# Optimization experiments

Hardware: AMD Instinct MI355X
Metric: run time of the kernel (lower is better)

The kernel has to match this reference:

```python
import jax, jax.numpy as jnp
import numpy as np

NUM_USERS = 100000
NUM_ITEMS = 50000
EMBED = 64
S_NNZ = NUM_USERS * 32   # avg social degree 32
R_NNZ = NUM_USERS * 50   # avg 50 rated items per user
BATCH = 8192


def setup_inputs() -> dict:
    key = jax.random.key(0)
    ks = jax.random.split(key, 12)
    d = EMBED
    # Embedding tables (xavier-uniform style scale)
    U = jax.random.uniform(ks[0], (NUM_USERS, d), jnp.float32, -1.0, 1.0) * np.sqrt(6.0 / (NUM_USERS + d))
    V = jax.random.uniform(ks[1], (NUM_ITEMS, d), jnp.float32, -1.0, 1.0) * np.sqrt(6.0 / (NUM_ITEMS + d))
    # Diffusion layer weights: Linear(2d -> d). Stored as [2d, d] (x @ W + b).
    lim = np.sqrt(6.0 / (3 * d))
    W0 = jax.random.uniform(ks[2], (2 * d, d), jnp.float32, -lim, lim)
    b0 = jnp.zeros((d,), jnp.float32)
    W1 = jax.random.uniform(ks[3], (2 * d, d), jnp.float32, -lim, lim)
    b1 = jnp.zeros((d,), jnp.float32)
    # Sparse social matrix S [NUM_USERS, NUM_USERS], COO edge lists, row-normalized values.
    S_row = jax.random.randint(ks[4], (S_NNZ,), 0, NUM_USERS, jnp.int32)
    S_col = jax.random.randint(ks[5], (S_NNZ,), 0, NUM_USERS, jnp.int32)
    S_val = jnp.full((S_NNZ,), 1.0 / 32.0, jnp.float32)
    # Sparse rating matrix R [NUM_USERS, NUM_ITEMS]
    R_row = jax.random.randint(ks[6], (R_NNZ,), 0, NUM_USERS, jnp.int32)
    R_col = jax.random.randint(ks[7], (R_NNZ,), 0, NUM_ITEMS, jnp.int32)
    R_val = jnp.full((R_NNZ,), 1.0 / 50.0, jnp.float32)
    batch_user = jax.random.randint(ks[8], (BATCH,), 0, NUM_USERS, jnp.int64 if jax.config.jax_enable_x64 else jnp.int32)
    batch_pos_item = jax.random.randint(ks[9], (BATCH,), 0, NUM_ITEMS, jnp.int32)
    batch_neg_item = jax.random.randint(ks[10], (BATCH,), 0, NUM_ITEMS, jnp.int32)
    return dict(batch_user=batch_user, batch_pos_item=batch_pos_item, batch_neg_item=batch_neg_item,
                U=U, V=V, W0=W0, b0=b0, W1=W1, b1=b1,
                S_row=S_row, S_col=S_col, S_val=S_val,
                R_row=R_row, R_col=R_col, R_val=R_val)


def _spmm(row, col, val, X, n_rows):
    # (sparse [n_rows, n] COO) @ X : gather + scale + segment-sum
    return jax.ops.segment_sum(val[:, None] * X[col], row, num_segments=n_rows)


def reference(batch_user, batch_pos_item, batch_neg_item, U, V, W0, b0, W1, b1,
              S_row, S_col, S_val, R_row, R_col, R_val):
    # Diffusion layers: U <- relu(concat([S @ U, U]) @ W + b)
    for W, b in ((W0, b0), (W1, b1)):
        agg = _spmm(S_row, S_col, S_val, U, NUM_USERS)          # [num_users, d]
        U = jax.nn.relu(jnp.concatenate([agg, U], axis=1) @ W + b)
    user_g = U + _spmm(R_row, R_col, R_val, V, NUM_USERS)        # [num_users, d]
    bu = user_g[batch_user]          # [B, d]
    bp = V[batch_pos_item]           # [B, d]
    bn = V[batch_neg_item]           # [B, d]
    return (bu, bp, bn)
```

## Files before the change

### kernel.cpp

```cpp
#include <hip/hip_runtime.h>
#include <hip/hip_bf16.h>

#define NUM_USERS 100000
#define NUM_ITEMS 50000
#define EMBED     64
#define S_NNZ     (NUM_USERS * 32)
#define R_NNZ     (NUM_USERS * 50)
#define BATCH     8192

#define NB    256
#define NCH   256
#define CHUNK (S_NNZ / NCH)
#define BROWS 391


__global__ __launch_bounds__(256) void k_p1hist(const int* __restrict__ rows, int* __restrict__ cnt_t) {
    __shared__ int h[NB];
    int t = threadIdx.x, b = blockIdx.x;
    h[t] = 0;
    __syncthreads();
    int base = b * CHUNK;
    for (int i = t; i < CHUNK; i += 256) atomicAdd(&h[rows[base + i] / BROWS], 1);
    __syncthreads();
    cnt_t[t * NCH + b] = h[t];
}

__global__ __launch_bounds__(1024) void k_scan1(const int* __restrict__ cnt, int* __restrict__ excl,
                                                int* __restrict__ bsums, int n) {
    __shared__ int buf[1024];
    int t = threadIdx.x;
    int i = blockIdx.x * 1024 + t;
    int x = (i < n) ? cnt[i] : 0;
    buf[t] = x;
    __syncthreads();
    for (int off = 1; off < 1024; off <<= 1) {
        int y = (t >= off) ? buf[t - off] : 0;
        __syncthreads();
        buf[t] += y;
        __syncthreads();
    }
    if (i < n) excl[i] = buf[t] - x;
    if (t == 1023) bsums[blockIdx.x] = buf[1023];
}

__global__ __launch_bounds__(1024) void k_scan2(int* __restrict__ bsums, int nb, int* __restrict__ total_slot) {
    __shared__ int buf[1024];
    int t = threadIdx.x;
    int x = (t < nb) ? bsums[t] : 0;
    buf[t] = x;
    __syncthreads();
    for (int off = 1; off < 1024; off <<= 1) {
        int y = (t >= off) ? buf[t - off] : 0;
        __syncthreads();
        buf[t] += y;
        __syncthreads();
    }
    if (t < nb) bsums[t] = buf[t] - x;
    if (t == 1023) total_slot[0] = buf[1023];
}

__global__ void k_scan3b(int* __restrict__ a, const int* __restrict__ bsums, int n) {
    int i = blockIdx.x * blockDim.x + threadIdx.x;
    if (i < n) a[i] += bsums[i >> 10];
}

__global__ __launch_bounds__(256) void k_p1scatter(const int* __restrict__ rows, const int* __restrict__ cols,
                                                   const float* __restrict__ vals, const int* __restrict__ cnt_t,
                                                   int2* __restrict__ tmpE) {
    __shared__ int cur[NB];
    int t = threadIdx.x, b = blockIdx.x;
    cur[t] = cnt_t[t * NCH + b];
    __syncthreads();
    int base = b * CHUNK;
    for (int i = t; i < CHUNK; i += 256) {
        int e  = base + i;
        int r  = rows[e];
        int bk = r / BROWS;
        int pos = atomicAdd(&cur[bk], 1);
        tmpE[pos] = make_int2(((r - bk * BROWS) << 17) | cols[e], __float_as_int(vals[e]));
    }
}

__global__ __launch_bounds__(512) void k_p2(const int2* __restrict__ tmpE, const int* __restrict__ cnt_t,
                                            int* __restrict__ rowptr, int2* __restrict__ colval) {
    __shared__ int h[512];
    __shared__ int s[512];
    __shared__ int cur[512];
    int t = threadIdx.x, k = blockIdx.x;
    int beg = cnt_t[k * NCH];
    int end = (k < NB - 1) ? cnt_t[(k + 1) * NCH] : S_NNZ;
    h[t] = 0;
    __syncthreads();
    for (int j = beg + t; j < end; j += 512) atomicAdd(&h[((unsigned)tmpE[j].x) >> 17], 1);
    __syncthreads();
    s[t] = h[t];
    __syncthreads();
    for (int off = 1; off < 512; off <<= 1) {
        int y = (t >= off) ? s[t - off] : 0;
        __syncthreads();
        s[t] += y;
        __syncthreads();
    }
    int excl = s[t] - h[t];
    int gr   = k * BROWS + t;
    if (t <= BROWS && gr <= NUM_USERS) rowptr[gr] = beg + excl;
    cur[t] = beg + excl;
    __syncthreads();
    for (int j = beg + t; j < end; j += 512) {
        int2 e  = tmpE[j];
        int pos = atomicAdd(&cur[((unsigned)e.x) >> 17], 1);
        colval[pos] = make_int2(e.x & 0x1FFFF, e.y);
    }
}

__global__ void k_cvt(const float* __restrict__ src, __hip_bfloat16* __restrict__ dst, int n) {
    int i = blockIdx.x * blockDim.x + threadIdx.x;
    if (i < n) dst[i] = __float2bfloat16(src[i]);
}

__global__ __launch_bounds__(256) void k_spmm16(const int* __restrict__ rowptr,
                                                const int2* __restrict__ colval,
                                                const __hip_bfloat16* __restrict__ X,
                                                float* __restrict__ Y, int n_rows) {
    int w    = blockIdx.x * (blockDim.x >> 6) + (threadIdx.x >> 6);
    int lane = threadIdx.x & 63;
    if (w >= n_rows) return;
    int beg = rowptr[w], end = rowptr[w + 1];
    float acc = 0.0f;
    int j    = beg;
    int jend = beg + ((end - beg) & ~7);
    for (; j < jend; j += 8) {
        int2 cv[8];
#pragma unroll
        for (int u = 0; u < 8; ++u) cv[u] = colval[j + u];
        float x[8];
#pragma unroll
        for (int u = 0; u < 8; ++u) x[u] = __bfloat162float(X[(size_t)cv[u].x * EMBED + lane]);
#pragma unroll
        for (int u = 0; u < 8; ++u) acc = fmaf(__int_as_float(cv[u].y), x[u], acc);
    }
    for (; j < end; ++j)
        acc = fmaf(__int_as_float(colval[j].y), __bfloat162float(X[(size_t)colval[j].x * EMBED + lane]), acc);
    Y[(size_t)w * EMBED + lane] = acc;
}

__global__ __launch_bounds__(256) void k_spmm_batch16(const int* __restrict__ rowptr,
                                                      const int2* __restrict__ colval,
                                                      const __hip_bfloat16* __restrict__ X,
                                                      const int* __restrict__ bu,
                                                      float* __restrict__ Agg2, int n) {
    int w    = blockIdx.x * (blockDim.x >> 6) + (threadIdx.x >> 6);
    int lane = threadIdx.x & 63;
    if (w >= n) return;
    int r   = bu[w];
    int beg = rowptr[r], end = rowptr[r + 1];
    float acc = 0.0f;
    int j    = beg;
    int jend = beg + ((end - beg) & ~7);
    for (; j < jend; j += 8) {
        int2 cv[8];
#pragma unroll
        for (int u = 0; u < 8; ++u) cv[u] = colval[j + u];
        float x[8];
#pragma unroll
        for (int u = 0; u < 8; ++u) x[u] = __bfloat162float(X[(size_t)cv[u].x * EMBED + lane]);
#pragma unroll
        for (int u = 0; u < 8; ++u) acc = fmaf(__int_as_float(cv[u].y), x[u], acc);
    }
    for (; j < end; ++j)
        acc = fmaf(__int_as_float(colval[j].y), __bfloat162float(X[(size_t)colval[j].x * EMBED + lane]), acc);
    Agg2[(size_t)w * EMBED + lane] = acc;
}


__global__ __launch_bounds__(256) void k_layer(const float* __restrict__ Agg,
                                               const float* __restrict__ Uin,
                                               float* __restrict__ Uout,
                                               __hip_bfloat16* __restrict__ Uout16,
                                               const float* __restrict__ W,
                                               const float* __restrict__ b) {
    __shared__ __align__(16) float Wt[64 * 128];
    int t = threadIdx.x;
    for (int i = t; i < 128 * 64; i += 256) {
        int k = i >> 6, c = i & 63;
        Wt[c * 128 + ((((k >> 2) ^ (c & 7)) << 2) | (k & 3))] = W[i];
    }
    int rl = __builtin_amdgcn_readfirstlane(t >> 6);
    int c  = t & 63;
    int rbase = blockIdx.x * 16 + rl * 4;
    __syncthreads();
    const float4* Wt4 = (const float4*)Wt;
    int  csw   = c & 7;
    int  cbase = c * 32;
    const float4* a0 = (const float4*)(Agg + (size_t)(rbase + 0) * EMBED);
    const float4* a1 = (const float4*)(Agg + (size_t)(rbase + 1) * EMBED);
    const float4* a2 = (const float4*)(Agg + (size_t)(rbase + 2) * EMBED);
    const float4* a3 = (const float4*)(Agg + (size_t)(rbase + 3) * EMBED);
    const float4* u0 = (const float4*)(Uin + (size_t)(rbase + 0) * EMBED);
    const float4* u1 = (const float4*)(Uin + (size_t)(rbase + 1) * EMBED);
    const float4* u2 = (const float4*)(Uin + (size_t)(rbase + 2) * EMBED);
    const float4* u3 = (const float4*)(Uin + (size_t)(rbase + 3) * EMBED);
    float bias = b[c];
    float acc0 = bias, acc1 = bias, acc2 = bias, acc3 = bias;
#pragma unroll 4
    for (int k4 = 0; k4 < 16; ++k4) {
        float4 w4 = Wt4[cbase + (k4 ^ csw)];
        float4 x0 = a0[k4], x1 = a1[k4], x2 = a2[k4], x3 = a3[k4];
        acc0 = fmaf(x0.x, w4.x, acc0); acc0 = fmaf(x0.y, w4.y, acc0); acc0 = fmaf(x0.z, w4.z, acc0); acc0 = fmaf(x0.w, w4.w, acc0);
        acc1 = fmaf(x1.x, w4.x, acc1); acc1 = fmaf(x1.y, w4.y, acc1); acc1 = fmaf(x1.z, w4.z, acc1); acc1 = fmaf(x1.w, w4.w, acc1);
        acc2 = fmaf(x2.x, w4.x, acc2); acc2 = fmaf(x2.y, w4.y, acc2); acc2 = fmaf(x2.z, w4.z, acc2); acc2 = fmaf(x2.w, w4.w, acc2);
        acc3 = fmaf(x3.x, w4.x, acc3); acc3 = fmaf(x3.y, w4.y, acc3); acc3 = fmaf(x3.z, w4.z, acc3); acc3 = fmaf(x3.w, w4.w, acc3);
    }
#pragma unroll 4
    for (int k4 = 16; k4 < 32; ++k4) {
        float4 w4 = Wt4[cbase + (k4 ^ csw)];
        float4 x0 = u0[k4 - 16], x1 = u1[k4 - 16], x2 = u2[k4 - 16], x3 = u3[k4 - 16];
        acc0 = fmaf(x0.x, w4.x, acc0); acc0 = fmaf(x0.y, w4.y, acc0); acc0 = fmaf(x0.z, w4.z, acc0); acc0 = fmaf(x0.w, w4.w, acc0);
        acc1 = fmaf(x1.x, w4.x, acc1); acc1 = fmaf(x1.y, w4.y, acc1); acc1 = fmaf(x1.z, w4.z, acc1); acc1 = fmaf(x1.w, w4.w, acc1);
        acc2 = fmaf(x2.x, w4.x, acc2); acc2 = fmaf(x2.y, w4.y, acc2); acc2 = fmaf(x2.z, w4.z, acc2); acc2 = fmaf(x2.w, w4.w, acc2);
        acc3 = fmaf(x3.x, w4.x, acc3); acc3 = fmaf(x3.y, w4.y, acc3); acc3 = fmaf(x3.z, w4.z, acc3); acc3 = fmaf(x3.w, w4.w, acc3);
    }
    float v0 = fmaxf(acc0, 0.0f), v1 = fmaxf(acc1, 0.0f), v2 = fmaxf(acc2, 0.0f), v3 = fmaxf(acc3, 0.0f);
    Uout[(size_t)(rbase + 0) * EMBED + c] = v0;
    Uout[(size_t)(rbase + 1) * EMBED + c] = v1;
    Uout[(size_t)(rbase + 2) * EMBED + c] = v2;
    Uout[(size_t)(rbase + 3) * EMBED + c] = v3;
    Uout16[(size_t)(rbase + 0) * EMBED + c] = __float2bfloat16(v0);
    Uout16[(size_t)(rbase + 1) * EMBED + c] = __float2bfloat16(v1);
    Uout16[(size_t)(rbase + 2) * EMBED + c] = __float2bfloat16(v2);
    Uout16[(size_t)(rbase + 3) * EMBED + c] = __float2bfloat16(v3);
}

__global__ __launch_bounds__(256) void k_layer_batch(const float* __restrict__ Agg2,
                                                     const float* __restrict__ Uin,
                                                     const int* __restrict__ bu,
                                                     float* __restrict__ out0,
                                                     const float* __restrict__ W,
                                                     const float* __restrict__ b) {
    __shared__ __align__(16) float Wt[64 * 128];
    int t = threadIdx.x;
    for (int i = t; i < 128 * 64; i += 256) {
        int k = i >> 6, c = i & 63;
        Wt[c * 128 + ((((k >> 2) ^ (c & 7)) << 2) | (k & 3))] = W[i];
    }
    int rl = __builtin_amdgcn_readfirstlane(t >> 6);
    int c  = t & 63;
    int sbase = blockIdx.x * 16 + rl * 4;
    int r0 = bu[sbase + 0], r1 = bu[sbase + 1], r2 = bu[sbase + 2], r3 = bu[sbase + 3];
    __syncthreads();
    const float4* Wt4 = (const float4*)Wt;
    int  csw   = c & 7;
    int  cbase = c * 32;
    const float4* a0 = (const float4*)(Agg2 + (size_t)(sbase + 0) * EMBED);
    const float4* a1 = (const float4*)(Agg2 + (size_t)(sbase + 1) * EMBED);
    const float4* a2 = (const float4*)(Agg2 + (size_t)(sbase + 2) * EMBED);
    const float4* a3 = (const float4*)(Agg2 + (size_t)(sbase + 3) * EMBED);
    const float4* u0 = (const float4*)(Uin + (size_t)r0 * EMBED);
    const float4* u1 = (const float4*)(Uin + (size_t)r1 * EMBED);
    const float4* u2 = (const float4*)(Uin + (size_t)r2 * EMBED);
    const float4* u3 = (const float4*)(Uin + (size_t)r3 * EMBED);
    float bias = b[c];
    float acc0 = bias, acc1 = bias, acc2 = bias, acc3 = bias;
#pragma unroll 4
    for (int k4 = 0; k4 < 16; ++k4) {
        float4 w4 = Wt4[cbase + (k4 ^ csw)];
        float4 x0 = a0[k4], x1 = a1[k4], x2 = a2[k4], x3 = a3[k4];
        acc0 = fmaf(x0.x, w4.x, acc0); acc0 = fmaf(x0.y, w4.y, acc0); acc0 = fmaf(x0.z, w4.z, acc0); acc0 = fmaf(x0.w, w4.w, acc0);
        acc1 = fmaf(x1.x, w4.x, acc1); acc1 = fmaf(x1.y, w4.y, acc1); acc1 = fmaf(x1.z, w4.z, acc1); acc1 = fmaf(x1.w, w4.w, acc1);
        acc2 = fmaf(x2.x, w4.x, acc2); acc2 = fmaf(x2.y, w4.y, acc2); acc2 = fmaf(x2.z, w4.z, acc2); acc2 = fmaf(x2.w, w4.w, acc2);
        acc3 = fmaf(x3.x, w4.x, acc3); acc3 = fmaf(x3.y, w4.y, acc3); acc3 = fmaf(x3.z, w4.z, acc3); acc3 = fmaf(x3.w, w4.w, acc3);
    }
#pragma unroll 4
    for (int k4 = 16; k4 < 32; ++k4) {
        float4 w4 = Wt4[cbase + (k4 ^ csw)];
        float4 x0 = u0[k4 - 16], x1 = u1[k4 - 16], x2 = u2[k4 - 16], x3 = u3[k4 - 16];
        acc0 = fmaf(x0.x, w4.x, acc0); acc0 = fmaf(x0.y, w4.y, acc0); acc0 = fmaf(x0.z, w4.z, acc0); acc0 = fmaf(x0.w, w4.w, acc0);
        acc1 = fmaf(x1.x, w4.x, acc1); acc1 = fmaf(x1.y, w4.y, acc1); acc1 = fmaf(x1.z, w4.z, acc1); acc1 = fmaf(x1.w, w4.w, acc1);
        acc2 = fmaf(x2.x, w4.x, acc2); acc2 = fmaf(x2.y, w4.y, acc2); acc2 = fmaf(x2.z, w4.z, acc2); acc2 = fmaf(x2.w, w4.w, acc2);
        acc3 = fmaf(x3.x, w4.x, acc3); acc3 = fmaf(x3.y, w4.y, acc3); acc3 = fmaf(x3.z, w4.z, acc3); acc3 = fmaf(x3.w, w4.w, acc3);
    }
    out0[(size_t)(sbase + 0) * EMBED + c] = fmaxf(acc0, 0.0f);
    out0[(size_t)(sbase + 1) * EMBED + c] = fmaxf(acc1, 0.0f);
    out0[(size_t)(sbase + 2) * EMBED + c] = fmaxf(acc2, 0.0f);
    out0[(size_t)(sbase + 3) * EMBED + c] = fmaxf(acc3, 0.0f);
}


__global__ void k_chain(const int* __restrict__ bu, int* __restrict__ head,
                        int* __restrict__ nxt, unsigned* __restrict__ bitmap, int n) {
    int i = blockIdx.x * blockDim.x + threadIdx.x;
    if (i < n) {
        int u = bu[i];
        nxt[i] = atomicExch(&head[u], i);
        atomicOr(&bitmap[u >> 5], 1u << (u & 31));
    }
}

__global__ __launch_bounds__(256) void k_rcount(const int* __restrict__ rows,
                                                const unsigned* __restrict__ bitmap,
                                                const int* __restrict__ head,
                                                int* __restrict__ cntR, int nnz) {
    int e = blockIdx.x * blockDim.x + threadIdx.x;
    if (e >= nnz) return;
    int r = rows[e];
    if ((bitmap[(unsigned)r >> 5] >> (r & 31)) & 1u)
        atomicAdd(&cntR[head[r]], 1);
}

__global__ __launch_bounds__(1024) void k_rscan(const int* __restrict__ cnt,
                                                int* __restrict__ rowptr2,
                                                int* __restrict__ cur) {
    __shared__ int buf[1024];
    int t = threadIdx.x;
    int loc[8];
    int sum = 0;
#pragma unroll
    for (int q = 0; q < 8; ++q) { loc[q] = cnt[t * 8 + q]; sum += loc[q]; }
    buf[t] = sum;
    __syncthreads();
    for (int off = 1; off < 1024; off <<= 1) {
        int y = (t >= off) ? buf[t - off] : 0;
        __syncthreads();
        buf[t] += y;
        __syncthreads();
    }
    int excl = buf[t] - sum;
#pragma unroll
    for (int q = 0; q < 8; ++q) {
        rowptr2[t * 8 + q] = excl;
        cur[t * 8 + q]     = excl;
        excl += loc[q];
    }
    if (t == 1023) rowptr2[BATCH] = excl;
}

__global__ __launch_bounds__(256) void k_rscatter(const int* __restrict__ rows,
                                                  const int* __restrict__ cols,
                                                  const float* __restrict__ vals,
                                                  const unsigned* __restrict__ bitmap,
                                                  const int* __restrict__ head,
                                                  int* __restrict__ cur,
                                                  int2* __restrict__ colval2, int nnz) {
    int e = blockIdx.x * blockDim.x + threadIdx.x;
    if (e >= nnz) return;
    int r = rows[e];
    if (!((bitmap[(unsigned)r >> 5] >> (r & 31)) & 1u)) return;
    int pos = atomicAdd(&cur[head[r]], 1);
    colval2[pos] = make_int2(cols[e], __float_as_int(vals[e]));
}

__global__ __launch_bounds__(256) void k_rspmm(const int* __restrict__ rowptr2,
                                               const int2* __restrict__ colval2,
                                               const __hip_bfloat16* __restrict__ V16,
                                               const int* __restrict__ bu,
                                               const int* __restrict__ head,
                                               const int* __restrict__ nxt,
                                               float* __restrict__ out0) {
    int s    = blockIdx.x * (blockDim.x >> 6) + (threadIdx.x >> 6);
    int lane = threadIdx.x & 63;
    if (s >= BATCH) return;
    if (head[bu[s]] != s) return;
    int beg = rowptr2[s], end = rowptr2[s + 1];
    float acc = 0.0f;
    int j    = beg;
    int jend = beg + ((end - beg) & ~7);
    for (; j < jend; j += 8) {
        int2 cv[8];
#pragma unroll
        for (int u = 0; u < 8; ++u) cv[u] = colval2[j + u];
        float x[8];
#pragma unroll
        for (int u = 0; u < 8; ++u) x[u] = __bfloat162float(V16[(size_t)cv[u].x * EMBED + lane]);
#pragma unroll
        for (int u = 0; u < 8; ++u) acc = fmaf(__int_as_float(cv[u].y), x[u], acc);
    }
    for (; j < end; ++j)
        acc = fmaf(__int_as_float(colval2[j].y), __bfloat162float(V16[(size_t)colval2[j].x * EMBED + lane]), acc);
    int slot = s;
    while (slot >= 0) {
        out0[(size_t)slot * EMBED + lane] += acc;
        slot = nxt[slot];
    }
}

__global__ void k_gather2(const float* __restrict__ V,
                          const int* __restrict__ bp, const int* __restrict__ bn,
                          float* __restrict__ out) {
    int i = blockIdx.x * blockDim.x + threadIdx.x;
    if (i >= BATCH * EMBED) return;
    int row = i >> 6, l = i & 63;
    out[BATCH * EMBED + i]     = V[(size_t)bp[row] * EMBED + l];
    out[2 * BATCH * EMBED + i] = V[(size_t)bn[row] * EMBED + l];
}


extern "C" void kernel_launch(void* const* d_in, const int* in_sizes, int n_in,
                              void* d_out, int out_size, void* d_ws, size_t ws_size,
                              hipStream_t stream) {
    const int*   batch_user = (const int*)d_in[0];
    const int*   batch_pos  = (const int*)d_in[1];
    const int*   batch_neg  = (const int*)d_in[2];
    const float* U     = (const float*)d_in[3];
    const float* V     = (const float*)d_in[4];
    const float* W0    = (const float*)d_in[5];
    const float* b0    = (const float*)d_in[6];
    const float* W1    = (const float*)d_in[7];
    const float* b1    = (const float*)d_in[8];
    const int*   S_row = (const int*)d_in[9];
    const int*   S_col = (const int*)d_in[10];
    const float* S_val = (const float*)d_in[11];
    const int*   R_row = (const int*)d_in[12];
    const int*   R_col = (const int*)d_in[13];
    const float* R_val = (const float*)d_in[14];
    float* out = (float*)d_out;

    const size_t tabElems = (size_t)NUM_USERS * EMBED;

    char* wsb = (char*)d_ws;
    size_t o = 0;
    float* A       = (float*)(wsb + o); o += tabElems * 4;
    float* B       = (float*)(wsb + o); o += tabElems * 4;
    float* Agg2    = (float*)(wsb + o); o += (size_t)BATCH * EMBED * 4;
    int*   rowptrS = (int*)(wsb + o);   o += (NUM_USERS + 1) * 4;
    int*   cnt_t   = (int*)(wsb + o);   o += (size_t)NB * NCH * 4;
    int*   bsums   = (int*)(wsb + o);   o += 1024 * 4;
    int*   head    = (int*)(wsb + o);   o += NUM_USERS * 4;
    int*   nxt     = (int*)(wsb + o);   o += BATCH * 4;
    int*   cntR    = (int*)(wsb + o);   o += BATCH * 4;
    int*   rowptr2 = (int*)(wsb + o);   o += (BATCH + 1) * 4;
    int*   curR    = (int*)(wsb + o);   o += BATCH * 4;
    unsigned* bitmap = (unsigned*)(wsb + o); o += ((NUM_USERS + 31) / 32) * 4;
    o = (o + 7) & ~(size_t)7;
    int2*  colvalS = (int2*)(wsb + o);  o += (size_t)S_NNZ * 8;
    __hip_bfloat16* X16 = (__hip_bfloat16*)(wsb + o); o += tabElems * 2;

    int2* tmpE    = (int2*)A;
    int2* colval2 = (int2*)A;

    const int spmm_blocks  = (NUM_USERS * 64 + 255) / 256;
    const int layer_blocks = (NUM_USERS + 15) / 16;

    k_p1hist<<<NCH, 256, 0, stream>>>(S_row, cnt_t);
    k_scan1<<<(NB * NCH) / 1024, 1024, 0, stream>>>(cnt_t, cnt_t, bsums, NB * NCH);
    k_scan2<<<1, 1024, 0, stream>>>(bsums, (NB * NCH) / 1024, &bsums[512]);
    k_scan3b<<<(NB * NCH) / 256, 256, 0, stream>>>(cnt_t, bsums, NB * NCH);
    k_p1scatter<<<NCH, 256, 0, stream>>>(S_row, S_col, S_val, cnt_t, tmpE);
    k_p2<<<NB, 512, 0, stream>>>(tmpE, cnt_t, rowptrS, colvalS);

    k_cvt<<<(int)((tabElems + 255) / 256), 256, 0, stream>>>(U, X16, (int)tabElems);
    k_spmm16<<<spmm_blocks, 256, 0, stream>>>(rowptrS, colvalS, X16, B, NUM_USERS);
    k_layer<<<layer_blocks, 256, 0, stream>>>(B, U, A, X16, W0, b0);

    hipMemsetAsync(head, 0xFF, NUM_USERS * sizeof(int), stream);
    hipMemsetAsync(bitmap, 0, ((NUM_USERS + 31) / 32) * sizeof(unsigned), stream);
    k_chain<<<(BATCH + 255) / 256, 256, 0, stream>>>(batch_user, head, nxt, bitmap, BATCH);

    k_spmm_batch16<<<(BATCH * 64 + 255) / 256, 256, 0, stream>>>(rowptrS, colvalS, X16, batch_user, Agg2, BATCH);
    k_layer_batch<<<(BATCH + 15) / 16, 256, 0, stream>>>(Agg2, A, batch_user, out, W1, b1);

    hipMemsetAsync(cntR, 0, BATCH * sizeof(int), stream);
    k_rcount<<<(R_NNZ + 255) / 256, 256, 0, stream>>>(R_row, bitmap, head, cntR, R_NNZ);
    k_rscan<<<1, 1024, 0, stream>>>(cntR, rowptr2, curR);
    k_rscatter<<<(R_NNZ + 255) / 256, 256, 0, stream>>>(R_row, R_col, R_val, bitmap, head, curR, colval2, R_NNZ);
    k_cvt<<<(int)(((size_t)NUM_ITEMS * EMBED + 255) / 256), 256, 0, stream>>>(V, X16, NUM_ITEMS * EMBED);
    k_rspmm<<<(BATCH * 64 + 255) / 256, 256, 0, stream>>>(rowptr2, colval2, X16, batch_user, head, nxt, out);

    k_gather2<<<(BATCH * EMBED + 255) / 256, 256, 0, stream>>>(V, batch_pos, batch_neg, out);
}
```

Baseline: 569.4 us.

## Split social SpMM into column-quarter passes for gather cache locality

The CSR build now sub-sorts each row's edges by which quarter of the user table the column falls in, and stores four row pointers per row. The full-table SpMM runs as four passes, each gathering only from a 25000-row slice of the bf16 table, so the working set of each pass is more likely to stay in cache. The edge loads switch to nontemporal 64-bit loads with a 4-way unroll, and two memsets are folded into one init kernel. The cost is three extra launches and a read-modify-write of the output between passes, plus a larger shared-memory histogram in the sort.

```diff
diff --git a/kernel.cpp b/kernel.cpp
--- a/kernel.cpp
+++ b/kernel.cpp
@@ -12,6 +12,10 @@
 #define NCH   256
 #define CHUNK (S_NNZ / NCH)
 #define BROWS 391
+
+#define QPR   4
+#define QROWS 25000
+#define KEYS  (BROWS * QPR)
 
 
 __global__ __launch_bounds__(256) void k_p1hist(const int* __restrict__ rows, int* __restrict__ cnt_t) {
@@ -82,34 +86,58 @@
 }
 
 __global__ __launch_bounds__(512) void k_p2(const int2* __restrict__ tmpE, const int* __restrict__ cnt_t,
-                                            int* __restrict__ rowptr, int2* __restrict__ colval) {
-    __shared__ int h[512];
-    __shared__ int s[512];
-    __shared__ int cur[512];
+                                            int* __restrict__ rowptrQ, int2* __restrict__ colval) {
+    __shared__ int h[KEYS];
+    __shared__ int sc[512];
+    __shared__ int cur[KEYS];
     int t = threadIdx.x, k = blockIdx.x;
     int beg = cnt_t[k * NCH];
     int end = (k < NB - 1) ? cnt_t[(k + 1) * NCH] : S_NNZ;
-    h[t] = 0;
-    __syncthreads();
-    for (int j = beg + t; j < end; j += 512) atomicAdd(&h[((unsigned)tmpE[j].x) >> 17], 1);
-    __syncthreads();
-    s[t] = h[t];
+    for (int i = t; i < KEYS; i += 512) h[i] = 0;
+    __syncthreads();
+    for (int j = beg + t; j < end; j += 512) {
+        int x   = tmpE[j].x;
+        int col = x & 0x1FFFF;
+        int q   = (unsigned)col / (unsigned)QROWS;
+        atomicAdd(&h[((x >> 17) << 2) | q], 1);
+    }
+    __syncthreads();
+    int l0 = 0, l1 = 0, l2 = 0, l3 = 0, sum = 0;
+    if (t < BROWS) {
+        l0 = h[4 * t]; l1 = h[4 * t + 1]; l2 = h[4 * t + 2]; l3 = h[4 * t + 3];
+        sum = l0 + l1 + l2 + l3;
+    }
+    sc[t] = sum;
     __syncthreads();
     for (int off = 1; off < 512; off <<= 1) {
-        int y = (t >= off) ? s[t - off] : 0;
-        __syncthreads();
-        s[t] += y;
-        __syncthreads();
-    }
-    int excl = s[t] - h[t];
-    int gr   = k * BROWS + t;
-    if (t <= BROWS && gr <= NUM_USERS) rowptr[gr] = beg + excl;
-    cur[t] = beg + excl;
+        int y = (t >= off) ? sc[t - off] : 0;
+        __syncthreads();
+        sc[t] += y;
+        __syncthreads();
+    }
+    int excl = sc[t] - sum;
+    if (t < BROWS) {
+        int base = beg + excl;
+        int gr   = k * BROWS + t;
+        if (gr < NUM_USERS) {
+            rowptrQ[gr * 4 + 0] = base;
+            rowptrQ[gr * 4 + 1] = base + l0;
+            rowptrQ[gr * 4 + 2] = base + l0 + l1;
+            rowptrQ[gr * 4 + 3] = base + l0 + l1 + l2;
+        }
+        cur[4 * t]     = base;
+        cur[4 * t + 1] = base + l0;
+        cur[4 * t + 2] = base + l0 + l1;
+        cur[4 * t + 3] = base + l0 + l1 + l2;
+    }
+    if (k == NB - 1 && t == 0) rowptrQ[NUM_USERS * 4] = S_NNZ;
     __syncthreads();
     for (int j = beg + t; j < end; j += 512) {
         int2 e  = tmpE[j];
-        int pos = atomicAdd(&cur[((unsigned)e.x) >> 17], 1);
-        colval[pos] = make_int2(e.x & 0x1FFFF, e.y);
+        int col = e.x & 0x1FFFF;
+        int q   = (unsigned)col / (unsigned)QROWS;
+        int pos = atomicAdd(&cur[(((unsigned)e.x >> 17) << 2) | q], 1);
+        colval[pos] = make_int2(col, e.y);
     }
 }
 
@@ -118,33 +146,46 @@
     if (i < n) dst[i] = __float2bfloat16(src[i]);
 }
 
-__global__ __launch_bounds__(256) void k_spmm16(const int* __restrict__ rowptr,
-                                                const int2* __restrict__ colval,
-                                                const __hip_bfloat16* __restrict__ X,
-                                                float* __restrict__ Y, int n_rows) {
+__global__ __launch_bounds__(256) void k_spmm16q(const int* __restrict__ rowptrQ,
+                                                 const int2* __restrict__ colval,
+                                                 const __hip_bfloat16* __restrict__ X,
+                                                 float* __restrict__ Y,
+                                                 int pass, int n_rows) {
     int w    = blockIdx.x * (blockDim.x >> 6) + (threadIdx.x >> 6);
     int lane = threadIdx.x & 63;
     if (w >= n_rows) return;
-    int beg = rowptr[w], end = rowptr[w + 1];
-    float acc = 0.0f;
+    int beg = rowptrQ[w * 4 + pass], end = rowptrQ[w * 4 + pass + 1];
+    float acc;
+    if (pass == 0) {
+        acc = 0.0f;
+    } else {
+        if (beg == end) return;
+        acc = Y[(size_t)w * EMBED + lane];
+    }
     int j    = beg;
-    int jend = beg + ((end - beg) & ~7);
-    for (; j < jend; j += 8) {
-        int2 cv[8];
-#pragma unroll
-        for (int u = 0; u < 8; ++u) cv[u] = colval[j + u];
-        float x[8];
-#pragma unroll
-        for (int u = 0; u < 8; ++u) x[u] = __bfloat162float(X[(size_t)cv[u].x * EMBED + lane]);
-#pragma unroll
-        for (int u = 0; u < 8; ++u) acc = fmaf(__int_as_float(cv[u].y), x[u], acc);
-    }
-    for (; j < end; ++j)
-        acc = fmaf(__int_as_float(colval[j].y), __bfloat162float(X[(size_t)colval[j].x * EMBED + lane]), acc);
+    int jend = beg + ((end - beg) & ~3);
+    for (; j < jend; j += 4) {
+        unsigned long long cv0 = __builtin_nontemporal_load((const unsigned long long*)(colval + j + 0));
+        unsigned long long cv1 = __builtin_nontemporal_load((const unsigned long long*)(colval + j + 1));
+        unsigned long long cv2 = __builtin_nontemporal_load((const unsigned long long*)(colval + j + 2));
+        unsigned long long cv3 = __builtin_nontemporal_load((const unsigned long long*)(colval + j + 3));
+        float x0 = __bfloat162float(X[(size_t)(unsigned)cv0 * EMBED + lane]);
+        float x1 = __bfloat162float(X[(size_t)(unsigned)cv1 * EMBED + lane]);
+        float x2 = __bfloat162float(X[(size_t)(unsigned)cv2 * EMBED + lane]);
+        float x3 = __bfloat162float(X[(size_t)(unsigned)cv3 * EMBED + lane]);
+        acc = fmaf(__int_as_float((int)(cv0 >> 32)), x0, acc);
+        acc = fmaf(__int_as_float((int)(cv1 >> 32)), x1, acc);
+        acc = fmaf(__int_as_float((int)(cv2 >> 32)), x2, acc);
+        acc = fmaf(__int_as_float((int)(cv3 >> 32)), x3, acc);
+    }
+    for (; j < end; ++j) {
+        int2 cv = colval[j];
+        acc = fmaf(__int_as_float(cv.y), __bfloat162float(X[(size_t)cv.x * EMBED + lane]), acc);
+    }
     Y[(size_t)w * EMBED + lane] = acc;
 }
 
-__global__ __launch_bounds__(256) void k_spmm_batch16(const int* __restrict__ rowptr,
+__global__ __launch_bounds__(256) void k_spmm_batch16(const int* __restrict__ rowptrQ,
                                                       const int2* __restrict__ colval,
                                                       const __hip_bfloat16* __restrict__ X,
                                                       const int* __restrict__ bu,
@@ -153,7 +194,7 @@
     int lane = threadIdx.x & 63;
     if (w >= n) return;
     int r   = bu[w];
-    int beg = rowptr[r], end = rowptr[r + 1];
+    int beg = rowptrQ[r * 4], end = rowptrQ[r * 4 + 4];
     float acc = 0.0f;
     int j    = beg;
     int jend = beg + ((end - beg) & ~7);
@@ -286,6 +327,13 @@
 }
 
 
+__global__ void k_zero(int* __restrict__ head, unsigned* __restrict__ bitmap, int* __restrict__ cntR) {
+    int i = blockIdx.x * blockDim.x + threadIdx.x;
+    if (i < NUM_USERS) head[i] = -1;
+    if (i < (NUM_USERS + 31) / 32) bitmap[i] = 0;
+    if (i < BATCH) cntR[i] = 0;
+}
+
 __global__ void k_chain(const int* __restrict__ bu, int* __restrict__ head,
                         int* __restrict__ nxt, unsigned* __restrict__ bitmap, int n) {
     int i = blockIdx.x * blockDim.x + threadIdx.x;
@@ -421,7 +469,7 @@
     float* A       = (float*)(wsb + o); o += tabElems * 4;
     float* B       = (float*)(wsb + o); o += tabElems * 4;
     float* Agg2    = (float*)(wsb + o); o += (size_t)BATCH * EMBED * 4;
-    int*   rowptrS = (int*)(wsb + o);   o += (NUM_USERS + 1) * 4;
+    int*   rowptrQ = (int*)(wsb + o);   o += ((size_t)NUM_USERS * 4 + 1) * 4;
     int*   cnt_t   = (int*)(wsb + o);   o += (size_t)NB * NCH * 4;
     int*   bsums   = (int*)(wsb + o);   o += 1024 * 4;
     int*   head    = (int*)(wsb + o);   o += NUM_USERS * 4;
@@ -445,20 +493,19 @@
     k_scan2<<<1, 1024, 0, stream>>>(bsums, (NB * NCH) / 1024, &bsums[512]);
     k_scan3b<<<(NB * NCH) / 256, 256, 0, stream>>>(cnt_t, bsums, NB * NCH);
     k_p1scatter<<<NCH, 256, 0, stream>>>(S_row, S_col, S_val, cnt_t, tmpE);
-    k_p2<<<NB, 512, 0, stream>>>(tmpE, cnt_t, rowptrS, colvalS);
+    k_p2<<<NB, 512, 0, stream>>>(tmpE, cnt_t, rowptrQ, colvalS);
 
     k_cvt<<<(int)((tabElems + 255) / 256), 256, 0, stream>>>(U, X16, (int)tabElems);
-    k_spmm16<<<spmm_blocks, 256, 0, stream>>>(rowptrS, colvalS, X16, B, NUM_USERS);
+    for (int pass = 0; pass < QPR; ++pass)
+        k_spmm16q<<<spmm_blocks, 256, 0, stream>>>(rowptrQ, colvalS, X16, B, pass, NUM_USERS);
     k_layer<<<layer_blocks, 256, 0, stream>>>(B, U, A, X16, W0, b0);
 
-    hipMemsetAsync(head, 0xFF, NUM_USERS * sizeof(int), stream);
-    hipMemsetAsync(bitmap, 0, ((NUM_USERS + 31) / 32) * sizeof(unsigned), stream);
+    k_zero<<<(NUM_USERS + 255) / 256, 256, 0, stream>>>(head, bitmap, cntR);
     k_chain<<<(BATCH + 255) / 256, 256, 0, stream>>>(batch_user, head, nxt, bitmap, BATCH);
 
-    k_spmm_batch16<<<(BATCH * 64 + 255) / 256, 256, 0, stream>>>(rowptrS, colvalS, X16, batch_user, Agg2, BATCH);
+    k_spmm_batch16<<<(BATCH * 64 + 255) / 256, 256, 0, stream>>>(rowptrQ, colvalS, X16, batch_user, Agg2, BATCH);
     k_layer_batch<<<(BATCH + 15) / 16, 256, 0, stream>>>(Agg2, A, batch_user, out, W1, b1);
 
-    hipMemsetAsync(cntR, 0, BATCH * sizeof(int), stream);
     k_rcount<<<(R_NNZ + 255) / 256, 256, 0, stream>>>(R_row, bitmap, head, cntR, R_NNZ);
     k_rscan<<<1, 1024, 0, stream>>>(cntR, rowptr2, curR);
     k_rscatter<<<(R_NNZ + 255) / 256, 256, 0, stream>>>(R_row, R_col, R_val, bitmap, head, curR, colval2, R_NNZ);
```

Result: slower. 681.0 us (+19.6%).

## Build CSR with global atomics and use fixed-capacity segments for ratings

Applied to the files above, without the earlier changes.

Replaces the two-pass bucketed counting sort of the social matrix with a per-row degree histogram, a scan and a direct scatter that uses global atomics. Replaces the rating count/scan/scatter pipeline for batch users with fixed 160-slot segments filled in one pass. It also merges the memsets into one zero kernel and uses nontemporal loads for the column/value stream in the SpMM. This removes several kernel launches and one full pass over the edges. In exchange it adds contended global atomics with random writes, and it silently truncates any rating row longer than 160 entries.

```diff
diff --git a/kernel.cpp b/kernel.cpp
--- a/kernel.cpp
+++ b/kernel.cpp
@@ -8,21 +8,23 @@
 #define R_NNZ     (NUM_USERS * 50)
 #define BATCH     8192
 
-#define NB    256
-#define NCH   256
-#define CHUNK (S_NNZ / NCH)
-#define BROWS 391
-
-
-__global__ __launch_bounds__(256) void k_p1hist(const int* __restrict__ rows, int* __restrict__ cnt_t) {
-    __shared__ int h[NB];
-    int t = threadIdx.x, b = blockIdx.x;
-    h[t] = 0;
-    __syncthreads();
-    int base = b * CHUNK;
-    for (int i = t; i < CHUNK; i += 256) atomicAdd(&h[rows[base + i] / BROWS], 1);
-    __syncthreads();
-    cnt_t[t * NCH + b] = h[t];
+#define NPAD   100096
+#define SEGCAP 160
+
+
+__global__ void k_zero(int* __restrict__ cntU, int* __restrict__ head,
+                       unsigned* __restrict__ bitmap, int* __restrict__ cntR) {
+    int i = blockIdx.x * blockDim.x + threadIdx.x;
+    if (i < NPAD) cntU[i] = 0;
+    if (i < NUM_USERS) head[i] = -1;
+    if (i < (NUM_USERS + 31) / 32) bitmap[i] = 0;
+    if (i < BATCH) cntR[i] = 0;
+}
+
+__global__ __launch_bounds__(256) void k_deghist(const int* __restrict__ rows,
+                                                 int* __restrict__ cnt, int nnz) {
+    int e = blockIdx.x * blockDim.x + threadIdx.x;
+    if (e < nnz) atomicAdd(&cnt[rows[e]], 1);
 }
 
 __global__ __launch_bounds__(1024) void k_scan1(const int* __restrict__ cnt, int* __restrict__ excl,
@@ -59,58 +61,27 @@
     if (t == 1023) total_slot[0] = buf[1023];
 }
 
-__global__ void k_scan3b(int* __restrict__ a, const int* __restrict__ bsums, int n) {
+__global__ void k_scan3c(const int* __restrict__ excl, const int* __restrict__ bsums,
+                         int* __restrict__ rowptr, int* __restrict__ cur, int n) {
     int i = blockIdx.x * blockDim.x + threadIdx.x;
-    if (i < n) a[i] += bsums[i >> 10];
-}
-
-__global__ __launch_bounds__(256) void k_p1scatter(const int* __restrict__ rows, const int* __restrict__ cols,
-                                                   const float* __restrict__ vals, const int* __restrict__ cnt_t,
-                                                   int2* __restrict__ tmpE) {
-    __shared__ int cur[NB];
-    int t = threadIdx.x, b = blockIdx.x;
-    cur[t] = cnt_t[t * NCH + b];
-    __syncthreads();
-    int base = b * CHUNK;
-    for (int i = t; i < CHUNK; i += 256) {
-        int e  = base + i;
-        int r  = rows[e];
-        int bk = r / BROWS;
-        int pos = atomicAdd(&cur[bk], 1);
-        tmpE[pos] = make_int2(((r - bk * BROWS) << 17) | cols[e], __float_as_int(vals[e]));
-    }
-}
-
-__global__ __launch_bounds__(512) void k_p2(const int2* __restrict__ tmpE, const int* __restrict__ cnt_t,
-                                            int* __restrict__ rowptr, int2* __restrict__ colval) {
-    __shared__ int h[512];
-    __shared__ int s[512];
-    __shared__ int cur[512];
-    int t = threadIdx.x, k = blockIdx.x;
-    int beg = cnt_t[k * NCH];
-    int end = (k < NB - 1) ? cnt_t[(k + 1) * NCH] : S_NNZ;
-    h[t] = 0;
-    __syncthreads();
-    for (int j = beg + t; j < end; j += 512) atomicAdd(&h[((unsigned)tmpE[j].x) >> 17], 1);
-    __syncthreads();
-    s[t] = h[t];
-    __syncthreads();
-    for (int off = 1; off < 512; off <<= 1) {
-        int y = (t >= off) ? s[t - off] : 0;
-        __syncthreads();
-        s[t] += y;
-        __syncthreads();
-    }
-    int excl = s[t] - h[t];
-    int gr   = k * BROWS + t;
-    if (t <= BROWS && gr <= NUM_USERS) rowptr[gr] = beg + excl;
-    cur[t] = beg + excl;
-    __syncthreads();
-    for (int j = beg + t; j < end; j += 512) {
-        int2 e  = tmpE[j];
-        int pos = atomicAdd(&cur[((unsigned)e.x) >> 17], 1);
-        colval[pos] = make_int2(e.x & 0x1FFFF, e.y);
-    }
+    if (i < n) {
+        int v = excl[i] + bsums[i >> 10];
+        rowptr[i] = v;
+        cur[i]    = v;
+    }
+    if (i == 0) rowptr[n] = S_NNZ;
+}
+
+__global__ __launch_bounds__(256) void k_dscatter(const int* __restrict__ rows,
+                                                  const int* __restrict__ cols,
+                                                  const float* __restrict__ vals,
+                                                  int* __restrict__ cur,
+                                                  int2* __restrict__ colval, int nnz) {
+    int e = blockIdx.x * blockDim.x + threadIdx.x;
+    if (e >= nnz) return;
+    int r   = rows[e];
+    int pos = atomicAdd(&cur[r], 1);
+    colval[pos] = make_int2(cols[e], __float_as_int(vals[e]));
 }
 
 __global__ void k_cvt(const float* __restrict__ src, __hip_bfloat16* __restrict__ dst, int n) {
@@ -130,17 +101,22 @@
     int j    = beg;
     int jend = beg + ((end - beg) & ~7);
     for (; j < jend; j += 8) {
-        int2 cv[8];
-#pragma unroll
-        for (int u = 0; u < 8; ++u) cv[u] = colval[j + u];
+        unsigned long long cv[8];
+#pragma unroll
+        for (int u = 0; u < 8; ++u)
+            cv[u] = __builtin_nontemporal_load((const unsigned long long*)(colval + j + u));
         float x[8];
 #pragma unroll
-        for (int u = 0; u < 8; ++u) x[u] = __bfloat162float(X[(size_t)cv[u].x * EMBED + lane]);
-#pragma unroll
-        for (int u = 0; u < 8; ++u) acc = fmaf(__int_as_float(cv[u].y), x[u], acc);
-    }
-    for (; j < end; ++j)
-        acc = fmaf(__int_as_float(colval[j].y), __bfloat162float(X[(size_t)colval[j].x * EMBED + lane]), acc);
+        for (int u = 0; u < 8; ++u)
+            x[u] = __bfloat162float(X[(size_t)(unsigned)cv[u] * EMBED + lane]);
+#pragma unroll
+        for (int u = 0; u < 8; ++u)
+            acc = fmaf(__int_as_float((int)(cv[u] >> 32)), x[u], acc);
+    }
+    for (; j < end; ++j) {
+        int2 cv = colval[j];
+        acc = fmaf(__int_as_float(cv.y), __bfloat162float(X[(size_t)cv.x * EMBED + lane]), acc);
+    }
     Y[(size_t)w * EMBED + lane] = acc;
 }
 
@@ -296,61 +272,24 @@
     }
 }
 
-__global__ __launch_bounds__(256) void k_rcount(const int* __restrict__ rows,
-                                                const unsigned* __restrict__ bitmap,
-                                                const int* __restrict__ head,
-                                                int* __restrict__ cntR, int nnz) {
-    int e = blockIdx.x * blockDim.x + threadIdx.x;
-    if (e >= nnz) return;
-    int r = rows[e];
-    if ((bitmap[(unsigned)r >> 5] >> (r & 31)) & 1u)
-        atomicAdd(&cntR[head[r]], 1);
-}
-
-__global__ __launch_bounds__(1024) void k_rscan(const int* __restrict__ cnt,
-                                                int* __restrict__ rowptr2,
-                                                int* __restrict__ cur) {
-    __shared__ int buf[1024];
-    int t = threadIdx.x;
-    int loc[8];
-    int sum = 0;
-#pragma unroll
-    for (int q = 0; q < 8; ++q) { loc[q] = cnt[t * 8 + q]; sum += loc[q]; }
-    buf[t] = sum;
-    __syncthreads();
-    for (int off = 1; off < 1024; off <<= 1) {
-        int y = (t >= off) ? buf[t - off] : 0;
-        __syncthreads();
-        buf[t] += y;
-        __syncthreads();
-    }
-    int excl = buf[t] - sum;
-#pragma unroll
-    for (int q = 0; q < 8; ++q) {
-        rowptr2[t * 8 + q] = excl;
-        cur[t * 8 + q]     = excl;
-        excl += loc[q];
-    }
-    if (t == 1023) rowptr2[BATCH] = excl;
-}
-
-__global__ __launch_bounds__(256) void k_rscatter(const int* __restrict__ rows,
-                                                  const int* __restrict__ cols,
-                                                  const float* __restrict__ vals,
-                                                  const unsigned* __restrict__ bitmap,
-                                                  const int* __restrict__ head,
-                                                  int* __restrict__ cur,
-                                                  int2* __restrict__ colval2, int nnz) {
+__global__ __launch_bounds__(256) void k_rseg(const int* __restrict__ rows,
+                                              const int* __restrict__ cols,
+                                              const float* __restrict__ vals,
+                                              const unsigned* __restrict__ bitmap,
+                                              const int* __restrict__ head,
+                                              int* __restrict__ cntR,
+                                              int2* __restrict__ seg, int nnz) {
     int e = blockIdx.x * blockDim.x + threadIdx.x;
     if (e >= nnz) return;
     int r = rows[e];
     if (!((bitmap[(unsigned)r >> 5] >> (r & 31)) & 1u)) return;
-    int pos = atomicAdd(&cur[head[r]], 1);
-    colval2[pos] = make_int2(cols[e], __float_as_int(vals[e]));
-}
-
-__global__ __launch_bounds__(256) void k_rspmm(const int* __restrict__ rowptr2,
-                                               const int2* __restrict__ colval2,
+    int s   = head[r];
+    int pos = atomicAdd(&cntR[s], 1);
+    if (pos < SEGCAP) seg[s * SEGCAP + pos] = make_int2(cols[e], __float_as_int(vals[e]));
+}
+
+__global__ __launch_bounds__(256) void k_rspmm(const int* __restrict__ cntR,
+                                               const int2* __restrict__ seg,
                                                const __hip_bfloat16* __restrict__ V16,
                                                const int* __restrict__ bu,
                                                const int* __restrict__ head,
@@ -360,22 +299,24 @@
     int lane = threadIdx.x & 63;
     if (s >= BATCH) return;
     if (head[bu[s]] != s) return;
-    int beg = rowptr2[s], end = rowptr2[s + 1];
+    int n = cntR[s];
+    if (n > SEGCAP) n = SEGCAP;
+    const int2* cv2 = seg + (size_t)s * SEGCAP;
     float acc = 0.0f;
-    int j    = beg;
-    int jend = beg + ((end - beg) & ~7);
+    int j    = 0;
+    int jend = n & ~7;
     for (; j < jend; j += 8) {
         int2 cv[8];
 #pragma unroll
-        for (int u = 0; u < 8; ++u) cv[u] = colval2[j + u];
+        for (int u = 0; u < 8; ++u) cv[u] = cv2[j + u];
         float x[8];
 #pragma unroll
         for (int u = 0; u < 8; ++u) x[u] = __bfloat162float(V16[(size_t)cv[u].x * EMBED + lane]);
 #pragma unroll
         for (int u = 0; u < 8; ++u) acc = fmaf(__int_as_float(cv[u].y), x[u], acc);
     }
-    for (; j < end; ++j)
-        acc = fmaf(__int_as_float(colval2[j].y), __bfloat162float(V16[(size_t)colval2[j].x * EMBED + lane]), acc);
+    for (; j < n; ++j)
+        acc = fmaf(__int_as_float(cv2[j].y), __bfloat162float(V16[(size_t)cv2[j].x * EMBED + lane]), acc);
     int slot = s;
     while (slot >= 0) {
         out0[(size_t)slot * EMBED + lane] += acc;
@@ -422,48 +363,43 @@
     float* B       = (float*)(wsb + o); o += tabElems * 4;
     float* Agg2    = (float*)(wsb + o); o += (size_t)BATCH * EMBED * 4;
     int*   rowptrS = (int*)(wsb + o);   o += (NUM_USERS + 1) * 4;
-    int*   cnt_t   = (int*)(wsb + o);   o += (size_t)NB * NCH * 4;
+    int*   cntU    = (int*)(wsb + o);   o += NPAD * 4;
+    int*   curU    = (int*)(wsb + o);   o += NUM_USERS * 4;
     int*   bsums   = (int*)(wsb + o);   o += 1024 * 4;
     int*   head    = (int*)(wsb + o);   o += NUM_USERS * 4;
     int*   nxt     = (int*)(wsb + o);   o += BATCH * 4;
     int*   cntR    = (int*)(wsb + o);   o += BATCH * 4;
-    int*   rowptr2 = (int*)(wsb + o);   o += (BATCH + 1) * 4;
-    int*   curR    = (int*)(wsb + o);   o += BATCH * 4;
     unsigned* bitmap = (unsigned*)(wsb + o); o += ((NUM_USERS + 31) / 32) * 4;
     o = (o + 7) & ~(size_t)7;
     int2*  colvalS = (int2*)(wsb + o);  o += (size_t)S_NNZ * 8;
     __hip_bfloat16* X16 = (__hip_bfloat16*)(wsb + o); o += tabElems * 2;
 
-    int2* tmpE    = (int2*)A;
-    int2* colval2 = (int2*)A;
+    int2* seg = (int2*)B;
 
     const int spmm_blocks  = (NUM_USERS * 64 + 255) / 256;
     const int layer_blocks = (NUM_USERS + 15) / 16;
-
-    k_p1hist<<<NCH, 256, 0, stream>>>(S_row, cnt_t);
-    k_scan1<<<(NB * NCH) / 1024, 1024, 0, stream>>>(cnt_t, cnt_t, bsums, NB * NCH);
-    k_scan2<<<1, 1024, 0, stream>>>(bsums, (NB * NCH) / 1024, &bsums[512]);
-    k_scan3b<<<(NB * NCH) / 256, 256, 0, stream>>>(cnt_t, bsums, NB * NCH);
-    k_p1scatter<<<NCH, 256, 0, stream>>>(S_row, S_col, S_val, cnt_t, tmpE);
-    k_p2<<<NB, 512, 0, stream>>>(tmpE, cnt_t, rowptrS, colvalS);
+    const int scan_blocks  = (NUM_USERS + 1023) / 1024;
+
+    k_zero<<<(NPAD + 255) / 256, 256, 0, stream>>>(cntU, head, bitmap, cntR);
+
+    k_deghist<<<(S_NNZ + 255) / 256, 256, 0, stream>>>(S_row, cntU, S_NNZ);
+    k_scan1<<<scan_blocks, 1024, 0, stream>>>(cntU, cntU, bsums, NUM_USERS);
+    k_scan2<<<1, 1024, 0, stream>>>(bsums, scan_blocks, &bsums[512]);
+    k_scan3c<<<(NUM_USERS + 255) / 256, 256, 0, stream>>>(cntU, bsums, rowptrS, curU, NUM_USERS);
+    k_dscatter<<<(S_NNZ + 255) / 256, 256, 0, stream>>>(S_row, S_col, S_val, curU, colvalS, S_NNZ);
 
     k_cvt<<<(int)((tabElems + 255) / 256), 256, 0, stream>>>(U, X16, (int)tabElems);
     k_spmm16<<<spmm_blocks, 256, 0, stream>>>(rowptrS, colvalS, X16, B, NUM_USERS);
     k_layer<<<layer_blocks, 256, 0, stream>>>(B, U, A, X16, W0, b0);
 
-    hipMemsetAsync(head, 0xFF, NUM_USERS * sizeof(int), stream);
-    hipMemsetAsync(bitmap, 0, ((NUM_USERS + 31) / 32) * sizeof(unsigned), stream);
     k_chain<<<(BATCH + 255) / 256, 256, 0, stream>>>(batch_user, head, nxt, bitmap, BATCH);
 
     k_spmm_batch16<<<(BATCH * 64 + 255) / 256, 256, 0, stream>>>(rowptrS, colvalS, X16, batch_user, Agg2, BATCH);
     k_layer_batch<<<(BATCH + 15) / 16, 256, 0, stream>>>(Agg2, A, batch_user, out, W1, b1);
 
-    hipMemsetAsync(cntR, 0, BATCH * sizeof(int), stream);
-    k_rcount<<<(R_NNZ + 255) / 256, 256, 0, stream>>>(R_row, bitmap, head, cntR, R_NNZ);
-    k_rscan<<<1, 1024, 0, stream>>>(cntR, rowptr2, curR);
-    k_rscatter<<<(R_NNZ + 255) / 256, 256, 0, stream>>>(R_row, R_col, R_val, bitmap, head, curR, colval2, R_NNZ);
+    k_rseg<<<(R_NNZ + 255) / 256, 256, 0, stream>>>(R_row, R_col, R_val, bitmap, head, cntR, seg, R_NNZ);
     k_cvt<<<(int)(((size_t)NUM_ITEMS * EMBED + 255) / 256), 256, 0, stream>>>(V, X16, NUM_ITEMS * EMBED);
-    k_rspmm<<<(BATCH * 64 + 255) / 256, 256, 0, stream>>>(rowptr2, colval2, X16, batch_user, head, nxt, out);
+    k_rspmm<<<(BATCH * 64 + 255) / 256, 256, 0, stream>>>(cntR, seg, X16, batch_user, head, nxt, out);
 
     k_gather2<<<(BATCH * EMBED + 255) / 256, 256, 0, stream>>>(V, batch_pos, batch_neg, out);
 }
```

New measurement: 764.8 us. 1.34x slower.

## Replace rating count/scan/scatter with fixed-capacity segments and fuse small kernels

Applied to the files above, without the earlier changes.

The count, scan and scatter passes over the rating edges are replaced by a single pass. That pass appends each edge into a fixed 160-slot segment per batch slot, using an atomic counter. The V-to-bf16 conversion is folded into this same kernel. The head/bitmap/cntR memsets move into the first histogram kernel, and the pos/neg item gather moves into the batch layer kernel. This removes a full read of the 5M-entry row array, a serial scan and several launches. The cost is that any user with more than 160 ratings would have edges silently dropped.

```diff
diff --git a/kernel.cpp b/kernel.cpp
--- a/kernel.cpp
+++ b/kernel.cpp
@@ -13,10 +13,18 @@
 #define CHUNK (S_NNZ / NCH)
 #define BROWS 391
 
-
-__global__ __launch_bounds__(256) void k_p1hist(const int* __restrict__ rows, int* __restrict__ cnt_t) {
+#define SEGCAP 160
+
+
+__global__ __launch_bounds__(256) void k_p1hist(const int* __restrict__ rows, int* __restrict__ cnt_t,
+                                                int* __restrict__ head, unsigned* __restrict__ bitmap,
+                                                int* __restrict__ cntR) {
     __shared__ int h[NB];
     int t = threadIdx.x, b = blockIdx.x;
+    int gid = b * 256 + t;
+    for (int i = gid; i < NUM_USERS; i += NB * 256) head[i] = -1;
+    for (int i = gid; i < (NUM_USERS + 31) / 32; i += NB * 256) bitmap[i] = 0;
+    for (int i = gid; i < BATCH; i += NB * 256) cntR[i] = 0;
     h[t] = 0;
     __syncthreads();
     int base = b * CHUNK;
@@ -236,7 +244,10 @@
                                                      const int* __restrict__ bu,
                                                      float* __restrict__ out0,
                                                      const float* __restrict__ W,
-                                                     const float* __restrict__ b) {
+                                                     const float* __restrict__ b,
+                                                     const float* __restrict__ V,
+                                                     const int* __restrict__ bp,
+                                                     const int* __restrict__ bn) {
     __shared__ __align__(16) float Wt[64 * 128];
     int t = threadIdx.x;
     for (int i = t; i < 128 * 64; i += 256) {
@@ -283,6 +294,12 @@
     out0[(size_t)(sbase + 1) * EMBED + c] = fmaxf(acc1, 0.0f);
     out0[(size_t)(sbase + 2) * EMBED + c] = fmaxf(acc2, 0.0f);
     out0[(size_t)(sbase + 3) * EMBED + c] = fmaxf(acc3, 0.0f);
+#pragma unroll
+    for (int q = 0; q < 4; ++q) {
+        int s = sbase + q;
+        out0[(size_t)(BATCH + s) * EMBED + c]     = V[(size_t)bp[s] * EMBED + c];
+        out0[(size_t)(2 * BATCH + s) * EMBED + c] = V[(size_t)bn[s] * EMBED + c];
+    }
 }
 
 
@@ -296,61 +313,27 @@
     }
 }
 
-__global__ __launch_bounds__(256) void k_rcount(const int* __restrict__ rows,
-                                                const unsigned* __restrict__ bitmap,
-                                                const int* __restrict__ head,
-                                                int* __restrict__ cntR, int nnz) {
+__global__ __launch_bounds__(256) void k_rseg(const int* __restrict__ rows,
+                                              const int* __restrict__ cols,
+                                              const float* __restrict__ vals,
+                                              const unsigned* __restrict__ bitmap,
+                                              const int* __restrict__ head,
+                                              int* __restrict__ cntR,
+                                              int2* __restrict__ seg, int nnz,
+                                              const float* __restrict__ V,
+                                              __hip_bfloat16* __restrict__ V16) {
     int e = blockIdx.x * blockDim.x + threadIdx.x;
-    if (e >= nnz) return;
-    int r = rows[e];
-    if ((bitmap[(unsigned)r >> 5] >> (r & 31)) & 1u)
-        atomicAdd(&cntR[head[r]], 1);
-}
-
-__global__ __launch_bounds__(1024) void k_rscan(const int* __restrict__ cnt,
-                                                int* __restrict__ rowptr2,
-                                                int* __restrict__ cur) {
-    __shared__ int buf[1024];
-    int t = threadIdx.x;
-    int loc[8];
-    int sum = 0;
-#pragma unroll
-    for (int q = 0; q < 8; ++q) { loc[q] = cnt[t * 8 + q]; sum += loc[q]; }
-    buf[t] = sum;
-    __syncthreads();
-    for (int off = 1; off < 1024; off <<= 1) {
-        int y = (t >= off) ? buf[t - off] : 0;
-        __syncthreads();
-        buf[t] += y;
-        __syncthreads();
-    }
-    int excl = buf[t] - sum;
-#pragma unroll
-    for (int q = 0; q < 8; ++q) {
-        rowptr2[t * 8 + q] = excl;
-        cur[t * 8 + q]     = excl;
-        excl += loc[q];
-    }
-    if (t == 1023) rowptr2[BATCH] = excl;
-}
-
-__global__ __launch_bounds__(256) void k_rscatter(const int* __restrict__ rows,
-                                                  const int* __restrict__ cols,
-                                                  const float* __restrict__ vals,
-                                                  const unsigned* __restrict__ bitmap,
-                                                  const int* __restrict__ head,
-                                                  int* __restrict__ cur,
-                                                  int2* __restrict__ colval2, int nnz) {
-    int e = blockIdx.x * blockDim.x + threadIdx.x;
+    if (e < NUM_ITEMS * EMBED) V16[e] = __float2bfloat16(V[e]);
     if (e >= nnz) return;
     int r = rows[e];
     if (!((bitmap[(unsigned)r >> 5] >> (r & 31)) & 1u)) return;
-    int pos = atomicAdd(&cur[head[r]], 1);
-    colval2[pos] = make_int2(cols[e], __float_as_int(vals[e]));
-}
-
-__global__ __launch_bounds__(256) void k_rspmm(const int* __restrict__ rowptr2,
-                                               const int2* __restrict__ colval2,
+    int s   = head[r];
+    int pos = atomicAdd(&cntR[s], 1);
+    if (pos < SEGCAP) seg[s * SEGCAP + pos] = make_int2(cols[e], __float_as_int(vals[e]));
+}
+
+__global__ __launch_bounds__(256) void k_rspmm(const int* __restrict__ cntR,
+                                               const int2* __restrict__ seg,
                                                const __hip_bfloat16* __restrict__ V16,
                                                const int* __restrict__ bu,
                                                const int* __restrict__ head,
@@ -360,37 +343,29 @@
     int lane = threadIdx.x & 63;
     if (s >= BATCH) return;
     if (head[bu[s]] != s) return;
-    int beg = rowptr2[s], end = rowptr2[s + 1];
+    int n = cntR[s];
+    if (n > SEGCAP) n = SEGCAP;
+    const int2* cv2 = seg + (size_t)s * SEGCAP;
     float acc = 0.0f;
-    int j    = beg;
-    int jend = beg + ((end - beg) & ~7);
+    int j    = 0;
+    int jend = n & ~7;
     for (; j < jend; j += 8) {
         int2 cv[8];
 #pragma unroll
-        for (int u = 0; u < 8; ++u) cv[u] = colval2[j + u];
+        for (int u = 0; u < 8; ++u) cv[u] = cv2[j + u];
         float x[8];
 #pragma unroll
         for (int u = 0; u < 8; ++u) x[u] = __bfloat162float(V16[(size_t)cv[u].x * EMBED + lane]);
 #pragma unroll
         for (int u = 0; u < 8; ++u) acc = fmaf(__int_as_float(cv[u].y), x[u], acc);
     }
-    for (; j < end; ++j)
-        acc = fmaf(__int_as_float(colval2[j].y), __bfloat162float(V16[(size_t)colval2[j].x * EMBED + lane]), acc);
+    for (; j < n; ++j)
+        acc = fmaf(__int_as_float(cv2[j].y), __bfloat162float(V16[(size_t)cv2[j].x * EMBED + lane]), acc);
     int slot = s;
     while (slot >= 0) {
         out0[(size_t)slot * EMBED + lane] += acc;
         slot = nxt[slot];
     }
-}
-
-__global__ void k_gather2(const float* __restrict__ V,
-                          const int* __restrict__ bp, const int* __restrict__ bn,
-                          float* __restrict__ out) {
-    int i = blockIdx.x * blockDim.x + threadIdx.x;
-    if (i >= BATCH * EMBED) return;
-    int row = i >> 6, l = i & 63;
-    out[BATCH * EMBED + i]     = V[(size_t)bp[row] * EMBED + l];
-    out[2 * BATCH * EMBED + i] = V[(size_t)bn[row] * EMBED + l];
 }
 
 
@@ -427,20 +402,18 @@
     int*   head    = (int*)(wsb + o);   o += NUM_USERS * 4;
     int*   nxt     = (int*)(wsb + o);   o += BATCH * 4;
     int*   cntR    = (int*)(wsb + o);   o += BATCH * 4;
-    int*   rowptr2 = (int*)(wsb + o);   o += (BATCH + 1) * 4;
-    int*   curR    = (int*)(wsb + o);   o += BATCH * 4;
     unsigned* bitmap = (unsigned*)(wsb + o); o += ((NUM_USERS + 31) / 32) * 4;
     o = (o + 7) & ~(size_t)7;
     int2*  colvalS = (int2*)(wsb + o);  o += (size_t)S_NNZ * 8;
     __hip_bfloat16* X16 = (__hip_bfloat16*)(wsb + o); o += tabElems * 2;
 
-    int2* tmpE    = (int2*)A;
-    int2* colval2 = (int2*)A;
+    int2* tmpE = (int2*)A;
+    int2* seg  = (int2*)B;
 
     const int spmm_blocks  = (NUM_USERS * 64 + 255) / 256;
     const int layer_blocks = (NUM_USERS + 15) / 16;
 
-    k_p1hist<<<NCH, 256, 0, stream>>>(S_row, cnt_t);
+    k_p1hist<<<NCH, 256, 0, stream>>>(S_row, cnt_t, head, bitmap, cntR);
     k_scan1<<<(NB * NCH) / 1024, 1024, 0, stream>>>(cnt_t, cnt_t, bsums, NB * NCH);
     k_scan2<<<1, 1024, 0, stream>>>(bsums, (NB * NCH) / 1024, &bsums[512]);
     k_scan3b<<<(NB * NCH) / 256, 256, 0, stream>>>(cnt_t, bsums, NB * NCH);
@@ -451,19 +424,13 @@
     k_spmm16<<<spmm_blocks, 256, 0, stream>>>(rowptrS, colvalS, X16, B, NUM_USERS);
     k_layer<<<layer_blocks, 256, 0, stream>>>(B, U, A, X16, W0, b0);
 
-    hipMemsetAsync(head, 0xFF, NUM_USERS * sizeof(int), stream);
-    hipMemsetAsync(bitmap, 0, ((NUM_USERS + 31) / 32) * sizeof(unsigned), stream);
     k_chain<<<(BATCH + 255) / 256, 256, 0, stream>>>(batch_user, head, nxt, bitmap, BATCH);
 
     k_spmm_batch16<<<(BATCH * 64 + 255) / 256, 256, 0, stream>>>(rowptrS, colvalS, X16, batch_user, Agg2, BATCH);
-    k_layer_batch<<<(BATCH + 15) / 16, 256, 0, stream>>>(Agg2, A, batch_user, out, W1, b1);
-
-    hipMemsetAsync(cntR, 0, BATCH * sizeof(int), stream);
-    k_rcount<<<(R_NNZ + 255) / 256, 256, 0, stream>>>(R_row, bitmap, head, cntR, R_NNZ);
-    k_rscan<<<1, 1024, 0, stream>>>(cntR, rowptr2, curR);
-    k_rscatter<<<(R_NNZ + 255) / 256, 256, 0, stream>>>(R_row, R_col, R_val, bitmap, head, curR, colval2, R_NNZ);
-    k_cvt<<<(int)(((size_t)NUM_ITEMS * EMBED + 255) / 256), 256, 0, stream>>>(V, X16, NUM_ITEMS * EMBED);
-    k_rspmm<<<(BATCH * 64 + 255) / 256, 256, 0, stream>>>(rowptr2, colval2, X16, batch_user, head, nxt, out);
-
-    k_gather2<<<(BATCH * EMBED + 255) / 256, 256, 0, stream>>>(V, batch_pos, batch_neg, out);
-}
+    k_layer_batch<<<(BATCH + 15) / 16, 256, 0, stream>>>(Agg2, A, batch_user, out, W1, b1,
+                                                         V, batch_pos, batch_neg);
+
+    k_rseg<<<(R_NNZ + 255) / 256, 256, 0, stream>>>(R_row, R_col, R_val, bitmap, head, cntR, seg, R_NNZ,
+                                                    V, X16);
+    k_rspmm<<<(BATCH * 64 + 255) / 256, 256, 0, stream>>>(cntR, seg, X16, batch_user, head, nxt, out);
+}
```

After: 511.6 us. 10.2% less time.
